# Kernel tuning notes

Measured on AMD Instinct MI355X. Metric: run time of the kernel, lower is better.

Reference implementation:

```python
import jax, jax.numpy as jnp
import numpy as np

B, N, NQ, D, H = 16, 1024, 1024, 512, 8
HD = D // H  # per-head kq dim and per-head v-output dim (64)


def setup_inputs() -> dict:
    key = jax.random.key(0)
    ks = jax.random.split(key, 7)
    s = 0.02  # small init like torch Linear default scale
    return {
        "x":   jax.random.normal(ks[0], (B, N, D), jnp.float32),
        "r":   jax.random.normal(ks[1], (B, N, D), jnp.float32),
        "x_q": jax.random.normal(ks[2], (B, NQ, D), jnp.float32),
        # per-head projection weights, torch Linear layout (out, in), stacked over heads
        "Wq": jax.random.normal(ks[3], (H, HD, D), jnp.float32) * s,
        "Wk": jax.random.normal(ks[4], (H, HD, D), jnp.float32) * s,
        "Wv": jax.random.normal(ks[5], (H, HD, D), jnp.float32) * s,  # applied AFTER attention
        "Wo": jax.random.normal(ks[6], (D, D), jnp.float32) * s,
    }


def reference(x, r, x_q, Wq, Wk, Wv, Wo):
    # AttentionAggregator.forward(x, r, x_q) -> MultiHeadAttention(q=x_q, k=x, v=r)
    qh = jnp.einsum('bnd,hed->bhne', x_q, Wq)            # (B,H,NQ,HD)
    kh = jnp.einsum('bmd,hed->bhme', x, Wk)              # (B,H,N,HD)
    scale = jnp.sqrt(jnp.float32(HD))                    # sqrt(d_k) with d_k = head_kq_dim_out
    scores = jnp.einsum('bhne,bhme->bhnm', qh, kh) / scale
    attn = jax.nn.softmax(scores, axis=-1)               # normalize=True path
    # NOTE: v (=r) is NOT projected before attention in the original module
    ctx = jnp.einsum('bhnm,bmd->bhnd', attn, r)          # (B,H,NQ,D)
    heads = jnp.einsum('bhnd,hed->bhne', ctx, Wv)        # (B,H,NQ,HD), per-head post-projection
    concat = heads.transpose(0, 2, 1, 3).reshape(B, NQ, H * HD)  # cat over heads, dim=-1
    return concat @ Wo.T                                 # head_o (post_process=True)
```

## Files before the change

kernel.cpp:

```cpp
#include <hip/hip_runtime.h>


#define B_  16
#define N_  1024
#define D_  512
#define M_  (B_ * N_)

typedef short short8 __attribute__((ext_vector_type(8)));
typedef float f32x4 __attribute__((ext_vector_type(4)));
typedef unsigned short ushort;
typedef unsigned int uint;

__device__ __forceinline__ ushort bf16rne(float f) {
  uint u = __float_as_uint(f);
  u += 0x7FFFu + ((u >> 16) & 1u);
  return (ushort)(u >> 16);
}
__device__ __forceinline__ uint bf16pk(float lo, float hi) {
  return (uint)bf16rne(lo) | ((uint)bf16rne(hi) << 16);
}
__device__ __forceinline__ void gload_lds16(const void* g, void* l) {
  __builtin_amdgcn_global_load_lds(
      (const __attribute__((address_space(1))) uint*)g,
      (__attribute__((address_space(3))) uint*)l, 16, 0, 0);
}
__device__ __forceinline__ float exp2_hw(float x) {
  float r;
  asm("v_exp_f32 %0, %1" : "=v"(r) : "v"(x));
  return r;
}
__device__ __forceinline__ uint cvtpk_bf16(float lo, float hi) {
  uint r;
  asm("v_cvt_pk_bf16_f32 %0, %1, %2" : "=v"(r) : "v"(lo), "v"(hi));
  return r;
}

union U4S8 { uint u[4]; short8 s; };

__global__ __launch_bounds__(256) void cast3_k(
    const float* __restrict__ s0, const float* __restrict__ s1,
    const float* __restrict__ s2, ushort* __restrict__ d, long n)
{
  const float* s = (blockIdx.y == 0) ? s0 : (blockIdx.y == 1) ? s1 : s2;
  ushort* dz = d + (long)blockIdx.y * n;
  long i = ((long)blockIdx.x * 256 + threadIdx.x) * 8;
  float4 v0 = *(const float4*)(s + i);
  float4 v1 = *(const float4*)(s + i + 4);
  uint4 o;
  o.x = bf16pk(v0.x, v0.y); o.y = bf16pk(v0.z, v0.w);
  o.z = bf16pk(v1.x, v1.y); o.w = bf16pk(v1.z, v1.w);
  *(uint4*)(dz + i) = o;
}

__global__ __launch_bounds__(256) void castW_k(
    const float* __restrict__ w0, const float* __restrict__ w1,
    const float* __restrict__ w2, const float* __restrict__ w3,
    ushort* __restrict__ d, long n)
{
  const int z = blockIdx.y;
  const float* s = (z == 0) ? w0 : (z == 1) ? w1 : (z == 2) ? w2 : w3;
  const float sc = (z == 0) ? 0.1803368801f : 1.f;
  ushort* dz = d + (long)z * n;
  long i = ((long)blockIdx.x * 256 + threadIdx.x) * 8;
  float4 v0 = *(const float4*)(s + i);
  float4 v1 = *(const float4*)(s + i + 4);
  uint4 o;
  o.x = bf16pk(v0.x * sc, v0.y * sc); o.y = bf16pk(v0.z * sc, v0.w * sc);
  o.z = bf16pk(v1.x * sc, v1.y * sc); o.w = bf16pk(v1.z * sc, v1.w * sc);
  *(uint4*)(dz + i) = o;
}

template <int MODE>
__global__ __launch_bounds__(256) void gemm_k(
    const ushort* __restrict__ Abase, const ushort* __restrict__ Wbase,
    void* __restrict__ C0, ushort* __restrict__ Vt)
{
  const long SB = (long)M_ * D_, WB = (long)D_ * D_;
  const int nwg = gridDim.x, per = nwg >> 3;
  const int wg = ((int)blockIdx.x & 7) * per + ((int)blockIdx.x >> 3);
  int z, bx, by;
  if constexpr (MODE == 0) { z = wg >> 9; bx = wg & 3; by = (wg & 511) >> 2; }
  else                     { z = 0;       bx = wg & 3; by = wg >> 2; }
  const ushort* A = Abase + z * SB;
  const ushort* W = Wbase + z * WB;

  __shared__ __align__(16) ushort Al[2][128 * 64];
  __shared__ __align__(16) ushort Bl[2][128 * 64];
  const int t = threadIdx.x, lane = t & 63, w = t >> 6;
  const int g = lane >> 4, lr = lane & 15;
  const int wr = w >> 1, wc = w & 1;
  const long m0 = (long)by * 128, n0 = (long)bx * 128;

  f32x4 acc[4][4] = {};

  auto STAGE = [&](int k0, int bufi) {
    #pragma unroll
    for (int u = 0; u < 4; ++u) {
      const int a = t * 16 + u * 4096;
      const int row = a >> 7, ch = (a >> 4) & 7;
      const int kk = k0 + ((ch ^ (row & 7)) << 3);
      gload_lds16(A + (m0 + row) * D_ + kk, (char*)Al[bufi] + a);
      gload_lds16(W + (n0 + row) * D_ + kk, (char*)Bl[bufi] + a);
    }
  };

  STAGE(0, 0);
  STAGE(64, 1);

  #pragma unroll
  for (int it = 0; it < 8; ++it) {
    const int cur = it & 1;
    if (it < 7) asm volatile("s_waitcnt vmcnt(8)" ::: "memory");
    else        asm volatile("s_waitcnt vmcnt(0)" ::: "memory");
    __builtin_amdgcn_s_barrier();

    short8 af[4][2], bf[4][2];
    #pragma unroll
    for (int mf = 0; mf < 4; ++mf)
      #pragma unroll
      for (int ks = 0; ks < 2; ++ks) {
        int row = wr * 64 + mf * 16 + lr;
        af[mf][ks] = *(const short8*)((const char*)Al[cur] + row * 128 + (((ks * 4 + g) ^ (row & 7)) << 4));
        row = wc * 64 + mf * 16 + lr;
        bf[mf][ks] = *(const short8*)((const char*)Bl[cur] + row * 128 + (((ks * 4 + g) ^ (row & 7)) << 4));
      }
    #pragma unroll
    for (int mf = 0; mf < 4; ++mf)
      #pragma unroll
      for (int nf = 0; nf < 4; ++nf)
        #pragma unroll
        for (int ks = 0; ks < 2; ++ks)
          acc[mf][nf] = __builtin_amdgcn_mfma_f32_16x16x32_bf16(
              af[mf][ks], bf[nf][ks], acc[mf][nf], 0, 0, 0);

    asm volatile("s_waitcnt lgkmcnt(0)" ::: "memory");
    __builtin_amdgcn_s_barrier();
    if (it < 6) STAGE((it + 2) * 64, cur);
  }

  if constexpr (MODE == 1) {
    float* C = (float*)C0;
    #pragma unroll
    for (int mf = 0; mf < 4; ++mf)
      #pragma unroll
      for (int nf = 0; nf < 4; ++nf)
        #pragma unroll
        for (int r = 0; r < 4; ++r)
          C[(m0 + wr * 64 + mf * 16 + g * 4 + r) * D_ + n0 + wc * 64 + nf * 16 + lr] =
              acc[mf][nf][r];
  } else {
    if (z < 2) {
      ushort* C = (ushort*)C0 + z * SB;
      #pragma unroll
      for (int mf = 0; mf < 4; ++mf)
        #pragma unroll
        for (int nf = 0; nf < 4; ++nf)
          #pragma unroll
          for (int r = 0; r < 4; ++r)
            C[(m0 + wr * 64 + mf * 16 + g * 4 + r) * D_ + n0 + wc * 64 + nf * 16 + lr] =
                bf16rne(acc[mf][nf][r]);
    } else {
      const int hh = (int)(n0 >> 6) + wc;
      #pragma unroll
      for (int mf = 0; mf < 4; ++mf) {
        const long m = m0 + wr * 64 + mf * 16 + g * 4;
        const int bb = (int)(m >> 10);
        const int kv = (int)(m & 1023);
        #pragma unroll
        for (int nf = 0; nf < 4; ++nf) {
          const int c = nf * 16 + lr;
          ushort4 o4;
          o4.x = bf16rne(acc[mf][nf][0]); o4.y = bf16rne(acc[mf][nf][1]);
          o4.z = bf16rne(acc[mf][nf][2]); o4.w = bf16rne(acc[mf][nf][3]);
          *(ushort4*)&Vt[((long)(bb * 8 + hh) * 64 + c) * (long)N_ + kv] = o4;
        }
      }
    }
  }
}

__global__ __launch_bounds__(256) void attn_mfma(
    const ushort* __restrict__ Q, const ushort* __restrict__ K,
    const ushort* __restrict__ Vt, ushort* __restrict__ Hd)
{
  __shared__ __align__(16) ushort Kl[2][64 * 64];
  __shared__ __align__(16) ushort Vl[2][64 * 64];
  const int t = threadIdx.x, lane = t & 63, w = t >> 6;
  const int g = lane >> 4, lr = lane & 15;
  const int bid = blockIdx.x;
  const int z = bid & 127, b = z >> 3, h = z & 7;
  const int qbase = (bid >> 7) * 128 + w * 32;

  short8 qf[2][2];
  #pragma unroll
  for (int nf = 0; nf < 2; ++nf)
    #pragma unroll
    for (int ks = 0; ks < 2; ++ks)
      qf[nf][ks] = *(const short8*)(Q + (long)(b * N_ + qbase + nf * 16 + lr) * D_ + h * 64 + ks * 32 + g * 8);

  f32x4 o[2][4] = {};
  float lsum[2] = {0.f, 0.f};

  const ushort* Kz = K + (long)b * N_ * D_ + h * 64;
  const ushort* Vz = Vt + (long)z * 64 * N_;

  auto STAGE = [&](int kt, int bufi) {
    #pragma unroll
    for (int u = 0; u < 2; ++u) {
      const int a = t * 16 + u * 4096;
      const int row = a >> 7, ch = (a >> 4) & 7;
      const int cc = (ch ^ (row & 7)) << 3;
      gload_lds16(Kz + (long)(kt * 64 + row) * D_ + cc, (char*)Kl[bufi] + a);
      gload_lds16(Vz + (long)row * N_ + kt * 64 + cc, (char*)Vl[bufi] + a);
    }
  };

  STAGE(0, 0);
  __syncthreads();

  for (int kt = 0; kt < 16; ++kt) {
    const int cur = kt & 1;
    if (kt < 15) STAGE(kt + 1, cur ^ 1);

    f32x4 s[4][2] = {};
    #pragma unroll
    for (int mf = 0; mf < 4; ++mf) {
      short8 kf[2];
      #pragma unroll
      for (int ks = 0; ks < 2; ++ks) {
        const int row = mf * 16 + lr;
        kf[ks] = *(const short8*)((const char*)Kl[cur] + row * 128 + (((ks * 4 + g) ^ (row & 7)) << 4));
      }
      #pragma unroll
      for (int nf = 0; nf < 2; ++nf)
        #pragma unroll
        for (int ks = 0; ks < 2; ++ks)
          s[mf][nf] = __builtin_amdgcn_mfma_f32_16x16x32_bf16(kf[ks], qf[nf][ks], s[mf][nf], 0, 0, 0);
    }

    short8 pa[2][2];
    #pragma unroll
    for (int nf = 0; nf < 2; ++nf) {
      uint Apk[4], Bpk[4];
      #pragma unroll
      for (int mf = 0; mf < 4; ++mf) {
        const float e0 = exp2_hw(s[mf][nf][0]);
        const float e1 = exp2_hw(s[mf][nf][1]);
        const float e2 = exp2_hw(s[mf][nf][2]);
        const float e3 = exp2_hw(s[mf][nf][3]);
        lsum[nf] += (e0 + e1) + (e2 + e3);
        Apk[mf] = cvtpk_bf16(e0, e1);
        Bpk[mf] = cvtpk_bf16(e2, e3);
      }
      asm("v_permlane32_swap_b32 %0, %1" : "+v"(Apk[0]), "+v"(Apk[1]));
      asm("v_permlane16_swap_b32 %0, %1" : "+v"(Apk[0]), "+v"(Apk[1]));
      asm("v_permlane32_swap_b32 %0, %1" : "+v"(Bpk[0]), "+v"(Bpk[1]));
      asm("v_permlane16_swap_b32 %0, %1" : "+v"(Bpk[0]), "+v"(Bpk[1]));
      asm("v_permlane32_swap_b32 %0, %1" : "+v"(Apk[2]), "+v"(Apk[3]));
      asm("v_permlane16_swap_b32 %0, %1" : "+v"(Apk[2]), "+v"(Apk[3]));
      asm("v_permlane32_swap_b32 %0, %1" : "+v"(Bpk[2]), "+v"(Bpk[3]));
      asm("v_permlane16_swap_b32 %0, %1" : "+v"(Bpk[2]), "+v"(Bpk[3]));
      U4S8 u0, u1;
      u0.u[0] = Apk[0]; u0.u[1] = Bpk[0]; u0.u[2] = Apk[1]; u0.u[3] = Bpk[1];
      u1.u[0] = Apk[2]; u1.u[1] = Bpk[2]; u1.u[2] = Apk[3]; u1.u[3] = Bpk[3];
      pa[nf][0] = u0.s;
      pa[nf][1] = u1.s;
    }

    #pragma unroll
    for (int ks = 0; ks < 2; ++ks) {
      short8 vb[4];
      #pragma unroll
      for (int nf = 0; nf < 4; ++nf) {
        const int row = nf * 16 + lr;
        vb[nf] = *(const short8*)((const char*)Vl[cur] + row * 128 + (((ks * 4 + g) ^ (row & 7)) << 4));
      }
      #pragma unroll
      for (int mf = 0; mf < 2; ++mf)
        #pragma unroll
        for (int nf = 0; nf < 4; ++nf)
          o[mf][nf] = __builtin_amdgcn_mfma_f32_16x16x32_bf16(pa[mf][ks], vb[nf], o[mf][nf], 0, 0, 0);
    }
    __syncthreads();
  }

  #pragma unroll
  for (int nf = 0; nf < 2; ++nf) {
    lsum[nf] += __shfl_xor(lsum[nf], 16);
    lsum[nf] += __shfl_xor(lsum[nf], 32);
  }

  #pragma unroll
  for (int mf = 0; mf < 2; ++mf)
    #pragma unroll
    for (int r = 0; r < 4; ++r) {
      const float inv = 1.f / __shfl(lsum[mf], g * 4 + r);
      const long grow = (long)b * N_ + qbase + mf * 16 + g * 4 + r;
      #pragma unroll
      for (int nf = 0; nf < 4; ++nf)
        Hd[grow * D_ + h * 64 + nf * 16 + lr] = bf16rne(o[mf][nf][r] * inv);
    }
}

extern "C" void kernel_launch(void* const* d_in, const int* in_sizes, int n_in,
                              void* d_out, int out_size, void* d_ws, size_t ws_size,
                              hipStream_t stream) {
  const float* x   = (const float*)d_in[0];
  const float* r   = (const float*)d_in[1];
  const float* x_q = (const float*)d_in[2];
  const float* Wq  = (const float*)d_in[3];
  const float* Wk  = (const float*)d_in[4];
  const float* Wv  = (const float*)d_in[5];
  const float* Wo  = (const float*)d_in[6];

  const long SBe = (long)M_ * D_;
  const long WBe = (long)D_ * D_;
  ushort* xqb = (ushort*)d_ws;
  ushort* xb  = xqb + SBe;
  ushort* rb  = xb  + SBe;
  ushort* Qb  = rb  + SBe;
  ushort* Kb  = Qb  + SBe;
  ushort* Vtb = Kb  + SBe;
  ushort* Wqb = Vtb + SBe;
  ushort* Hdb = xqb;

  dim3 blk(256);
  cast3_k<<<dim3(4096, 3), blk, 0, stream>>>(x_q, x, r, xqb, SBe);
  castW_k<<<dim3(128, 4),  blk, 0, stream>>>(Wq, Wk, Wv, Wo, Wqb, WBe);

  gemm_k<0><<<dim3(1536), blk, 0, stream>>>(xqb, Wqb, Qb, Vtb);

  attn_mfma<<<dim3(1024), blk, 0, stream>>>(Qb, Kb, Vtb, Hdb);

  gemm_k<1><<<dim3(512), blk, 0, stream>>>(Hdb, Wqb + 3 * WBe, d_out, nullptr);
}
```

Before: 245.7 us.

## Fuse fp32-to-bf16 input cast into projection GEMM; MFMA row sums in attention

Removes the separate kernel that cast x_q, x and r to bf16. The projection GEMM now loads fp32 activations into registers, converts them and writes them to LDS, double-buffered alongside the async weight loads. This saves writing and re-reading three bf16 activation copies through HBM, but the GEMM now fetches twice the A bytes and needs more registers. Separately, the attention kernel computes softmax row sums with an extra MFMA against a ones vector instead of scalar adds and shuffles, wraps its MFMA blocks in s_setprio, and the V-transpose store now uses packed hardware bf16 conversion.

```diff
diff --git a/kernel.cpp b/kernel.cpp
--- a/kernel.cpp
+++ b/kernel.cpp
@@ -36,21 +36,6 @@
 }
 
 union U4S8 { uint u[4]; short8 s; };
-
-__global__ __launch_bounds__(256) void cast3_k(
-    const float* __restrict__ s0, const float* __restrict__ s1,
-    const float* __restrict__ s2, ushort* __restrict__ d, long n)
-{
-  const float* s = (blockIdx.y == 0) ? s0 : (blockIdx.y == 1) ? s1 : s2;
-  ushort* dz = d + (long)blockIdx.y * n;
-  long i = ((long)blockIdx.x * 256 + threadIdx.x) * 8;
-  float4 v0 = *(const float4*)(s + i);
-  float4 v1 = *(const float4*)(s + i + 4);
-  uint4 o;
-  o.x = bf16pk(v0.x, v0.y); o.y = bf16pk(v0.z, v0.w);
-  o.z = bf16pk(v1.x, v1.y); o.w = bf16pk(v1.z, v1.w);
-  *(uint4*)(dz + i) = o;
-}
 
 __global__ __launch_bounds__(256) void castW_k(
     const float* __restrict__ w0, const float* __restrict__ w1,
@@ -72,8 +57,10 @@
 
 template <int MODE>
 __global__ __launch_bounds__(256) void gemm_k(
-    const ushort* __restrict__ Abase, const ushort* __restrict__ Wbase,
-    void* __restrict__ C0, ushort* __restrict__ Vt)
+    const float* __restrict__ Af0, const float* __restrict__ Af1,
+    const float* __restrict__ Af2, const ushort* __restrict__ Abf,
+    const ushort* __restrict__ Wbase, void* __restrict__ C0,
+    ushort* __restrict__ Vt)
 {
   const long SB = (long)M_ * D_, WB = (long)D_ * D_;
   const int nwg = gridDim.x, per = nwg >> 3;
@@ -81,8 +68,7 @@
   int z, bx, by;
   if constexpr (MODE == 0) { z = wg >> 9; bx = wg & 3; by = (wg & 511) >> 2; }
   else                     { z = 0;       bx = wg & 3; by = wg >> 2; }
-  const ushort* A = Abase + z * SB;
-  const ushort* W = Wbase + z * WB;
+  const ushort* W = (MODE == 0) ? Wbase + z * WB : Wbase;
 
   __shared__ __align__(16) ushort Al[2][128 * 64];
   __shared__ __align__(16) ushort Bl[2][128 * 64];
@@ -93,27 +79,17 @@
 
   f32x4 acc[4][4] = {};
 
-  auto STAGE = [&](int k0, int bufi) {
+  auto LOADW = [&](int k0, int bufi) {
     #pragma unroll
     for (int u = 0; u < 4; ++u) {
       const int a = t * 16 + u * 4096;
       const int row = a >> 7, ch = (a >> 4) & 7;
       const int kk = k0 + ((ch ^ (row & 7)) << 3);
-      gload_lds16(A + (m0 + row) * D_ + kk, (char*)Al[bufi] + a);
       gload_lds16(W + (n0 + row) * D_ + kk, (char*)Bl[bufi] + a);
     }
   };
 
-  STAGE(0, 0);
-  STAGE(64, 1);
-
-  #pragma unroll
-  for (int it = 0; it < 8; ++it) {
-    const int cur = it & 1;
-    if (it < 7) asm volatile("s_waitcnt vmcnt(8)" ::: "memory");
-    else        asm volatile("s_waitcnt vmcnt(0)" ::: "memory");
-    __builtin_amdgcn_s_barrier();
-
+  auto COMPUTE = [&](int cur) {
     short8 af[4][2], bf[4][2];
     #pragma unroll
     for (int mf = 0; mf < 4; ++mf)
@@ -132,10 +108,84 @@
         for (int ks = 0; ks < 2; ++ks)
           acc[mf][nf] = __builtin_amdgcn_mfma_f32_16x16x32_bf16(
               af[mf][ks], bf[nf][ks], acc[mf][nf], 0, 0, 0);
-
+  };
+
+  if constexpr (MODE == 0) {
+    const float* A = (z == 0) ? Af0 : (z == 1) ? Af1 : Af2;
+
+    auto LOADA = [&](int k0, float4* rA) {
+      #pragma unroll
+      for (int u = 0; u < 4; ++u) {
+        const int a = t * 16 + u * 4096;
+        const int row = a >> 7, ch = (a >> 4) & 7;
+        const float* src = A + (m0 + row) * D_ + k0 + ch * 8;
+        rA[2 * u]     = *(const float4*)(src);
+        rA[2 * u + 1] = *(const float4*)(src + 4);
+      }
+    };
+    auto WRITEA = [&](const float4* rA, int bufi) {
+      #pragma unroll
+      for (int u = 0; u < 4; ++u) {
+        const int a = t * 16 + u * 4096;
+        const int row = a >> 7, ch = (a >> 4) & 7;
+        const int dst = row * 128 + (((ch) ^ (row & 7)) << 4);
+        uint4 o;
+        o.x = cvtpk_bf16(rA[2 * u].x, rA[2 * u].y);
+        o.y = cvtpk_bf16(rA[2 * u].z, rA[2 * u].w);
+        o.z = cvtpk_bf16(rA[2 * u + 1].x, rA[2 * u + 1].y);
+        o.w = cvtpk_bf16(rA[2 * u + 1].z, rA[2 * u + 1].w);
+        *(uint4*)((char*)Al[bufi] + dst) = o;
+      }
+    };
+
+    float4 rA0[8], rA1[8];
+    LOADA(0, rA0);  LOADW(0, 0);
+    LOADA(64, rA1); LOADW(64, 1);
+    asm volatile("s_waitcnt vmcnt(12)" ::: "memory");
+    WRITEA(rA0, 0);
     asm volatile("s_waitcnt lgkmcnt(0)" ::: "memory");
     __builtin_amdgcn_s_barrier();
-    if (it < 6) STAGE((it + 2) * 64, cur);
+
+    #pragma unroll
+    for (int it = 0; it < 8; ++it) {
+      const int cur = it & 1;
+      COMPUTE(cur);
+      asm volatile("s_waitcnt lgkmcnt(0)" ::: "memory");
+      __builtin_amdgcn_s_barrier();
+      if (it + 2 < 8) { LOADA((it + 2) * 64, cur ? rA1 : rA0); LOADW((it + 2) * 64, cur); }
+      if (it + 1 < 8) {
+        if (it + 2 < 8) asm volatile("s_waitcnt vmcnt(12)" ::: "memory");
+        else            asm volatile("s_waitcnt vmcnt(0)"  ::: "memory");
+        WRITEA(cur ? rA0 : rA1, cur ^ 1);
+        asm volatile("s_waitcnt lgkmcnt(0)" ::: "memory");
+        __builtin_amdgcn_s_barrier();
+      }
+    }
+  } else {
+    const ushort* A = Abf;
+    auto STAGE = [&](int k0, int bufi) {
+      #pragma unroll
+      for (int u = 0; u < 4; ++u) {
+        const int a = t * 16 + u * 4096;
+        const int row = a >> 7, ch = (a >> 4) & 7;
+        const int kk = k0 + ((ch ^ (row & 7)) << 3);
+        gload_lds16(A + (m0 + row) * D_ + kk, (char*)Al[bufi] + a);
+        gload_lds16(W + (n0 + row) * D_ + kk, (char*)Bl[bufi] + a);
+      }
+    };
+    STAGE(0, 0);
+    STAGE(64, 1);
+    #pragma unroll
+    for (int it = 0; it < 8; ++it) {
+      const int cur = it & 1;
+      if (it < 7) asm volatile("s_waitcnt vmcnt(8)" ::: "memory");
+      else        asm volatile("s_waitcnt vmcnt(0)" ::: "memory");
+      __builtin_amdgcn_s_barrier();
+      COMPUTE(cur);
+      asm volatile("s_waitcnt lgkmcnt(0)" ::: "memory");
+      __builtin_amdgcn_s_barrier();
+      if (it < 6) STAGE((it + 2) * 64, cur);
+    }
   }
 
   if constexpr (MODE == 1) {
@@ -169,10 +219,10 @@
         #pragma unroll
         for (int nf = 0; nf < 4; ++nf) {
           const int c = nf * 16 + lr;
-          ushort4 o4;
-          o4.x = bf16rne(acc[mf][nf][0]); o4.y = bf16rne(acc[mf][nf][1]);
-          o4.z = bf16rne(acc[mf][nf][2]); o4.w = bf16rne(acc[mf][nf][3]);
-          *(ushort4*)&Vt[((long)(bb * 8 + hh) * 64 + c) * (long)N_ + kv] = o4;
+          uint2 o2;
+          o2.x = cvtpk_bf16(acc[mf][nf][0], acc[mf][nf][1]);
+          o2.y = cvtpk_bf16(acc[mf][nf][2], acc[mf][nf][3]);
+          *(uint2*)&Vt[((long)(bb * 8 + hh) * 64 + c) * (long)N_ + kv] = o2;
         }
       }
     }
@@ -198,8 +248,10 @@
     for (int ks = 0; ks < 2; ++ks)
       qf[nf][ks] = *(const short8*)(Q + (long)(b * N_ + qbase + nf * 16 + lr) * D_ + h * 64 + ks * 32 + g * 8);
 
+  const short8 ones = {0x3F80, 0x3F80, 0x3F80, 0x3F80, 0x3F80, 0x3F80, 0x3F80, 0x3F80};
+
   f32x4 o[2][4] = {};
-  float lsum[2] = {0.f, 0.f};
+  f32x4 acc_l[2] = {};
 
   const ushort* Kz = K + (long)b * N_ * D_ + h * 64;
   const ushort* Vz = Vt + (long)z * 64 * N_;
@@ -223,6 +275,7 @@
     if (kt < 15) STAGE(kt + 1, cur ^ 1);
 
     f32x4 s[4][2] = {};
+    __builtin_amdgcn_s_setprio(1);
     #pragma unroll
     for (int mf = 0; mf < 4; ++mf) {
       short8 kf[2];
@@ -237,6 +290,7 @@
         for (int ks = 0; ks < 2; ++ks)
           s[mf][nf] = __builtin_amdgcn_mfma_f32_16x16x32_bf16(kf[ks], qf[nf][ks], s[mf][nf], 0, 0, 0);
     }
+    __builtin_amdgcn_s_setprio(0);
 
     short8 pa[2][2];
     #pragma unroll
@@ -248,7 +302,6 @@
         const float e1 = exp2_hw(s[mf][nf][1]);
         const float e2 = exp2_hw(s[mf][nf][2]);
         const float e3 = exp2_hw(s[mf][nf][3]);
-        lsum[nf] += (e0 + e1) + (e2 + e3);
         Apk[mf] = cvtpk_bf16(e0, e1);
         Bpk[mf] = cvtpk_bf16(e2, e3);
       }
@@ -267,6 +320,7 @@
       pa[nf][1] = u1.s;
     }
 
+    __builtin_amdgcn_s_setprio(1);
     #pragma unroll
     for (int ks = 0; ks < 2; ++ks) {
       short8 vb[4];
@@ -276,25 +330,22 @@
         vb[nf] = *(const short8*)((const char*)Vl[cur] + row * 128 + (((ks * 4 + g) ^ (row & 7)) << 4));
       }
       #pragma unroll
-      for (int mf = 0; mf < 2; ++mf)
+      for (int mf = 0; mf < 2; ++mf) {
         #pragma unroll
         for (int nf = 0; nf < 4; ++nf)
           o[mf][nf] = __builtin_amdgcn_mfma_f32_16x16x32_bf16(pa[mf][ks], vb[nf], o[mf][nf], 0, 0, 0);
-    }
+        acc_l[mf] = __builtin_amdgcn_mfma_f32_16x16x32_bf16(pa[mf][ks], ones, acc_l[mf], 0, 0, 0);
+      }
+    }
+    __builtin_amdgcn_s_setprio(0);
     __syncthreads();
   }
 
   #pragma unroll
-  for (int nf = 0; nf < 2; ++nf) {
-    lsum[nf] += __shfl_xor(lsum[nf], 16);
-    lsum[nf] += __shfl_xor(lsum[nf], 32);
-  }
-
-  #pragma unroll
   for (int mf = 0; mf < 2; ++mf)
     #pragma unroll
     for (int r = 0; r < 4; ++r) {
-      const float inv = 1.f / __shfl(lsum[mf], g * 4 + r);
+      const float inv = 1.f / acc_l[mf][r];
       const long grow = (long)b * N_ + qbase + mf * 16 + g * 4 + r;
       #pragma unroll
       for (int nf = 0; nf < 4; ++nf)
@@ -315,22 +366,19 @@
 
   const long SBe = (long)M_ * D_;
   const long WBe = (long)D_ * D_;
-  ushort* xqb = (ushort*)d_ws;
-  ushort* xb  = xqb + SBe;
-  ushort* rb  = xb  + SBe;
-  ushort* Qb  = rb  + SBe;
+  ushort* Qb  = (ushort*)d_ws;
   ushort* Kb  = Qb  + SBe;
   ushort* Vtb = Kb  + SBe;
-  ushort* Wqb = Vtb + SBe;
-  ushort* Hdb = xqb;
+  ushort* Hdb = Vtb + SBe;
+  ushort* Wqb = Hdb + SBe;
 
   dim3 blk(256);
-  cast3_k<<<dim3(4096, 3), blk, 0, stream>>>(x_q, x, r, xqb, SBe);
-  castW_k<<<dim3(128, 4),  blk, 0, stream>>>(Wq, Wk, Wv, Wo, Wqb, WBe);
-
-  gemm_k<0><<<dim3(1536), blk, 0, stream>>>(xqb, Wqb, Qb, Vtb);
+  castW_k<<<dim3(128, 4), blk, 0, stream>>>(Wq, Wk, Wv, Wo, Wqb, WBe);
+
+  gemm_k<0><<<dim3(1536), blk, 0, stream>>>(x_q, x, r, nullptr, Wqb, Qb, Vtb);
 
   attn_mfma<<<dim3(1024), blk, 0, stream>>>(Qb, Kb, Vtb, Hdb);
 
-  gemm_k<1><<<dim3(512), blk, 0, stream>>>(Hdb, Wqb + 3 * WBe, d_out, nullptr);
-}
+  gemm_k<1><<<dim3(512), blk, 0, stream>>>(nullptr, nullptr, nullptr, Hdb,
+                                           Wqb + 3 * WBe, d_out, nullptr);
+}
```

After: 241.7 us. No clear change (-1.6%).
